# Optimization experiments

Hardware: AMD Instinct MI355X
Metric: run time of the kernel (lower is better)

The kernel has to match this reference:

```python
import jax, jax.numpy as jnp
import numpy as np

K = 3  # kernel size (hardcoded in module defaults; padding=1, stride=1, dilation=1)


def conv2d(x, w, b, pad=1):
    # x: [B,C,H,W], w: [O,C,kh,kw]
    out = jax.lax.conv_general_dilated(
        x, w, window_strides=(1, 1), padding=[(pad, pad), (pad, pad)],
        dimension_numbers=("NCHW", "OIHW", "NCHW"))
    return out + b[None, :, None, None]


def _bilinear_sample(img, py, px):
    # img: [C,H,W]; py, px: [K*K,Ho,Wo] float sample coords.
    # Zero-padded bilinear sampling (matches torchvision deform_conv2d):
    # each of the 4 corner taps contributes 0 if it lies outside the image.
    H, W = img.shape[1], img.shape[2]
    y0 = jnp.floor(py)
    x0 = jnp.floor(px)
    y1, x1 = y0 + 1.0, x0 + 1.0
    wy1 = py - y0
    wy0 = 1.0 - wy1
    wx1 = px - x0
    wx0 = 1.0 - wx1

    def corner(y, x):
        yi = jnp.clip(y.astype(jnp.int32), 0, H - 1)
        xi = jnp.clip(x.astype(jnp.int32), 0, W - 1)
        valid = ((y >= 0) & (y <= H - 1) & (x >= 0) & (x <= W - 1))
        return img[:, yi, xi] * valid.astype(img.dtype)[None]  # [C,K*K,Ho,Wo]

    return (corner(y0, x0) * (wy0 * wx0)[None]
            + corner(y0, x1) * (wy0 * wx1)[None]
            + corner(y1, x0) * (wy1 * wx0)[None]
            + corner(y1, x1) * (wy1 * wx1)[None])


def setup_inputs() -> dict:
    key = jax.random.key(0)
    ks = jax.random.split(key, 4)
    B, C, O, H, W = 8, 128, 256, 96, 96
    x = jax.random.normal(ks[0], (B, C, H, W), dtype=jnp.float32)
    # scale offset/mask conv weights so learned offsets stay a few pixels
    offset_w = jax.random.normal(ks[1], (2 * K * K, C, K, K), dtype=jnp.float32) * 0.01
    offset_b = jnp.zeros((2 * K * K,), dtype=jnp.float32)
    mask_w = jax.random.normal(ks[2], (K * K, C, K, K), dtype=jnp.float32) * 0.05
    mask_b = jnp.zeros((K * K,), dtype=jnp.float32)
    weight = jax.random.normal(ks[3], (O, C, K, K), dtype=jnp.float32) * 0.05
    bias = jnp.zeros((O,), dtype=jnp.float32)
    return {"x": x, "offset_w": offset_w, "offset_b": offset_b,
            "mask_w": mask_w, "mask_b": mask_b, "weight": weight, "bias": bias}


def reference(x, offset_w, offset_b, mask_w, mask_b, weight, bias):
    B, C, H, W = x.shape
    O = weight.shape[0]
    pad = 1
    offset = conv2d(x, offset_w, offset_b, pad)              # [B,2*K*K,H,W]
    mask = jax.nn.sigmoid(conv2d(x, mask_w, mask_b, pad))    # [B,K*K,H,W]
    Ho, Wo = offset.shape[2], offset.shape[3]

    # base sampling grid: output pixel - pad + kernel tap position
    kh, kw = jnp.meshgrid(jnp.arange(K), jnp.arange(K), indexing="ij")
    kh = kh.reshape(-1).astype(x.dtype)  # [K*K]
    kw = kw.reshape(-1).astype(x.dtype)
    base_y = (jnp.arange(Ho, dtype=x.dtype)[None, :, None] - pad
              + kh[:, None, None])                           # [K*K,Ho,1]
    base_x = (jnp.arange(Wo, dtype=x.dtype)[None, None, :] - pad
              + kw[:, None, None])                           # [K*K,1,Wo]

    # torchvision layout: channel 2k = y-offset, 2k+1 = x-offset for tap k
    off = offset.reshape(B, K * K, 2, Ho, Wo)
    py = base_y[None] + off[:, :, 0]                         # [B,K*K,Ho,Wo]
    px = base_x[None] + off[:, :, 1]

    samples = jax.vmap(_bilinear_sample)(x, py, px)          # [B,C,K*K,Ho,Wo]
    w_flat = weight.reshape(O, C, K * K)
    out = jnp.einsum("bckhw,bkhw,ock->bohw", samples, mask, w_flat)
    return out + bias[None, :, None, None]
```

## Files before the change

### kernel.cpp

```cpp
#include <hip/hip_runtime.h>

#define CIN 128
#define COUT 256
#define IH 96
#define IW 96
#define NB 8
#define HW (IH*IW)
#define NPIX (NB*HW)
#define AST 136
#define BLK_PER_IMG (HW/64)

typedef __attribute__((ext_vector_type(8))) short short8;
typedef __attribute__((ext_vector_type(4))) float floatx4;

static __device__ __forceinline__ short f2bf(float f) {
  unsigned int u = __builtin_bit_cast(unsigned int, f);
  u = u + 0x7fffu + ((u >> 16) & 1u);
  return (short)(u >> 16);
}
static __device__ __forceinline__ float bf2f(short s) {
  unsigned int u = ((unsigned int)(unsigned short)s) << 16;
  return __builtin_bit_cast(float, u);
}

struct Corner {
  float w00, w01, w10, w11;
  const short *r00, *r01, *r10, *r11;
};

static __device__ __forceinline__ Corner corner_setup(float py, float px, float mk,
                                                      const short* xtb, int choff) {
  Corner c;
  float y0f = floorf(py), x0f = floorf(px);
  float wy1 = py - y0f, wx1 = px - x0f;
  float wy0 = 1.f - wy1, wx0 = 1.f - wx1;
  bool vy0 = (y0f >= 0.f) && (y0f <= (float)(IH - 1));
  bool vy1 = (y0f + 1.f >= 0.f) && (y0f + 1.f <= (float)(IH - 1));
  bool vx0 = (x0f >= 0.f) && (x0f <= (float)(IW - 1));
  bool vx1 = (x0f + 1.f >= 0.f) && (x0f + 1.f <= (float)(IW - 1));
  int iy0 = min(max((int)y0f, 0), IH - 1);
  int iy1 = min(max((int)y0f + 1, 0), IH - 1);
  int ix0 = min(max((int)x0f, 0), IW - 1);
  int ix1 = min(max((int)x0f + 1, 0), IW - 1);
  c.w00 = wy0 * wx0 * mk * ((vy0 && vx0) ? 1.f : 0.f);
  c.w01 = wy0 * wx1 * mk * ((vy0 && vx1) ? 1.f : 0.f);
  c.w10 = wy1 * wx0 * mk * ((vy1 && vx0) ? 1.f : 0.f);
  c.w11 = wy1 * wx1 * mk * ((vy1 && vx1) ? 1.f : 0.f);
  c.r00 = xtb + (size_t)(iy0 * IW + ix0) * 128 + choff;
  c.r01 = xtb + (size_t)(iy0 * IW + ix1) * 128 + choff;
  c.r10 = xtb + (size_t)(iy1 * IW + ix0) * 128 + choff;
  c.r11 = xtb + (size_t)(iy1 * IW + ix1) * 128 + choff;
  return c;
}

static __device__ __forceinline__ short8 interp8(short8 s00, short8 s01,
                                                 short8 s10, short8 s11,
                                                 const Corner& c) {
  short8 o;
  #pragma unroll
  for (int j = 0; j < 8; ++j) {
    float v = c.w00 * bf2f(s00[j]) + c.w01 * bf2f(s01[j])
            + c.w10 * bf2f(s10[j]) + c.w11 * bf2f(s11[j]);
    o[j] = f2bf(v);
  }
  return o;
}

__global__ void prep_weights(const float* __restrict__ weight,
                             const float* __restrict__ offset_w,
                             const float* __restrict__ mask_w,
                             short* __restrict__ Bt2f,
                             short* __restrict__ Bt1f) {
  int idx = blockIdx.x * 256 + threadIdx.x;
  const int n2 = 9 * 4 * 16 * 512;
  if (idx < n2) {
    int e = idx & 7, lane = (idx >> 3) & 63;
    int g = idx >> 9;
    int nl = g & 15, kq = (g >> 4) & 3, tap = g >> 6;
    int o = nl * 16 + (lane & 15);
    int c = kq * 32 + (lane >> 4) * 8 + e;
    Bt2f[idx] = f2bf(weight[(o * CIN + c) * 9 + tap]);
  } else {
    int j = idx - n2;
    if (j < 9 * 4 * 2 * 512) {
      int e = j & 7, lane = (j >> 3) & 63;
      int g = j >> 9;
      int nl = g & 1, kq = (g >> 1) & 3, tap = g >> 3;
      int n = nl * 16 + (lane & 15);
      int c = kq * 32 + (lane >> 4) * 8 + e;
      float v = 0.f;
      if (n < 27)
        v = (n < 18) ? offset_w[(n * CIN + c) * 9 + tap]
                     : mask_w[((n - 18) * CIN + c) * 9 + tap];
      Bt1f[j] = f2bf(v);
    }
  }
}

__global__ __launch_bounds__(256, 8)
void transpose_x(const float* __restrict__ x, short* __restrict__ xt) {
  __shared__ short tile[64 * 130];
  const int tid = threadIdx.x;
  const int lane = tid & 63;
  const int wv = tid >> 6;
  const int p0 = blockIdx.x * 64;
  const int b = p0 / HW;
  const int hw0 = p0 % HW;
  const float* xb = x + (size_t)b * CIN * HW + hw0;

  #pragma unroll
  for (int i = 0; i < 32; ++i) {
    int c = wv + i * 4;
    tile[lane * 130 + c] = f2bf(xb[(size_t)c * HW + lane]);
  }
  __syncthreads();

  unsigned int* dst = (unsigned int*)(xt + ((size_t)b * HW + hw0) * 128);
  #pragma unroll
  for (int i = 0; i < 16; ++i) {
    int idx = i * 256 + tid;
    int px = idx >> 6, cw = idx & 63;
    unsigned int lo = (unsigned short)tile[px * 130 + 2 * cw];
    unsigned int hi = (unsigned short)tile[px * 130 + 2 * cw + 1];
    dst[idx] = lo | (hi << 16);
  }
}

__global__ __launch_bounds__(256, 4)
void offmask_kernel(const short* __restrict__ xt,
                    const short* __restrict__ Bt1f,
                    const float* __restrict__ offset_b,
                    const float* __restrict__ mask_b,
                    float* __restrict__ pmt) {
  const int tid  = threadIdx.x;
  const int lane = tid & 63;
  const int wv   = tid >> 6;
  const int q    = lane >> 4;
  const int m    = lane & 15;
  const int blk  = blockIdx.x;
  const int l    = (blk & 7) * BLK_PER_IMG + (blk >> 3);
  const int p0   = l * 64;
  const int b    = p0 / HW;
  const int p    = p0 + wv * 16 + m;
  const int hw   = p % HW;
  const int h    = hw / IW, w_ = hw % IW;
  const short* xtb = xt + (size_t)b * HW * 128;

  floatx4 acc0 = (floatx4){0.f, 0.f, 0.f, 0.f};
  floatx4 acc1 = (floatx4){0.f, 0.f, 0.f, 0.f};

  for (int tap = 0; tap < 9; ++tap) {
    const int kh = tap / 3, kw = tap % 3;
    const int iy = h + kh - 1, ix = w_ + kw - 1;
    const bool vald = (iy >= 0 && iy < IH && ix >= 0 && ix < IW);
    const size_t pbase = vald ? (size_t)(iy * IW + ix) * 128 : 0;

    short8 a[4], bb0[4], bb1[4];
    #pragma unroll
    for (int kq = 0; kq < 4; ++kq)
      a[kq] = *(const short8*)(xtb + pbase + kq * 32 + q * 8);
    #pragma unroll
    for (int kq = 0; kq < 4; ++kq) {
      bb0[kq] = *(const short8*)(Bt1f + (size_t)((tap * 4 + kq) * 2 + 0) * 512 + lane * 8);
      bb1[kq] = *(const short8*)(Bt1f + (size_t)((tap * 4 + kq) * 2 + 1) * 512 + lane * 8);
    }
    #pragma unroll
    for (int kq = 0; kq < 4; ++kq) {
      short8 av = a[kq];
      if (!vald) av = (short8){0, 0, 0, 0, 0, 0, 0, 0};
      acc0 = __builtin_amdgcn_mfma_f32_16x16x32_bf16(av, bb0[kq], acc0, 0, 0, 0);
      acc1 = __builtin_amdgcn_mfma_f32_16x16x32_bf16(av, bb1[kq], acc1, 0, 0, 0);
    }
  }

  #pragma unroll
  for (int nl = 0; nl < 2; ++nl) {
    floatx4 ac = nl ? acc1 : acc0;
    int ch = nl * 16 + m;
    if (ch < 18) {
      int tap = ch >> 1, plane = ch & 1;
      float cb = offset_b[ch];
      #pragma unroll
      for (int r = 0; r < 4; ++r) {
        int pp = p0 + wv * 16 + q * 4 + r;
        int hwp = pp % HW;
        float base = plane ? (float)(hwp % IW + tap % 3 - 1)
                           : (float)(hwp / IW + tap / 3 - 1);
        pmt[(size_t)(plane * 9 + tap) * NPIX + pp] = ac[r] + cb + base;
      }
    } else if (ch < 27) {
      int tap = ch - 18;
      float cb = mask_b[tap];
      #pragma unroll
      for (int r = 0; r < 4; ++r) {
        int pp = p0 + wv * 16 + q * 4 + r;
        float v = ac[r] + cb;
        pmt[(size_t)(18 + tap) * NPIX + pp] = 1.f / (1.f + expf(-v));
      }
    }
  }
}

__global__ __launch_bounds__(256, 2)
void deform_main(const short* __restrict__ xt,
                 const short* __restrict__ Bt2f,
                 const float* __restrict__ pmt,
                 const float* __restrict__ bias,
                 float* __restrict__ out) {
  __shared__ short Ald[2][64 * AST];

  const int tid  = threadIdx.x;
  const int lane = tid & 63;
  const int wv   = tid >> 6;
  const int q    = lane >> 4;
  const int m    = lane & 15;
  const int blk  = blockIdx.x;
  const int l    = (blk & 7) * BLK_PER_IMG + (blk >> 3);
  const int p0   = l * 64;
  const int b    = p0 / HW;
  const short* xtb = xt + (size_t)b * HW * 128;

  const int spx   = lane;
  const int p_s   = p0 + spx;
  const int choff = wv * 32;
  const int wsw   = (spx >> 1) & 7;
  const int rsw   = (m >> 1) & 7;
  short* const myrow0 = &Ald[0][spx * AST];
  short* const myrow1 = &Ald[1][spx * AST];

  floatx4 acc[4][4];
  #pragma unroll
  for (int i = 0; i < 4; ++i)
    #pragma unroll
    for (int j = 0; j < 4; ++j) acc[i][j] = (floatx4){0.f, 0.f, 0.f, 0.f};

  {
    float py = pmt[p_s];
    float px = pmt[(size_t)9 * NPIX + p_s];
    float mk = pmt[(size_t)18 * NPIX + p_s];
    Corner c = corner_setup(py, px, mk, xtb, choff);
    #pragma unroll
    for (int i = 0; i < 4; ++i) {
      short8 s00 = *(const short8*)(c.r00 + i * 8);
      short8 s01 = *(const short8*)(c.r01 + i * 8);
      short8 s10 = *(const short8*)(c.r10 + i * 8);
      short8 s11 = *(const short8*)(c.r11 + i * 8);
      *(short8*)(myrow0 + ((wv * 4 + i) ^ wsw) * 8) = interp8(s00, s01, s10, s11, c);
    }
  }
  float pyN = pmt[(size_t)1 * NPIX + p_s];
  float pxN = pmt[(size_t)10 * NPIX + p_s];
  float mkN = pmt[(size_t)19 * NPIX + p_s];
  __syncthreads();

  for (int tap = 0; tap < 9; ++tap) {
    const short* bufr = Ald[tap & 1];
    short* const roww = (tap & 1) ? myrow0 : myrow1;
    const bool nxt = (tap < 8);

    Corner c;
    if (nxt) c = corner_setup(pyN, pxN, mkN, xtb, choff);
    if (tap < 7) {
      pyN = pmt[(size_t)(tap + 2) * NPIX + p_s];
      pxN = pmt[(size_t)(tap + 11) * NPIX + p_s];
      mkN = pmt[(size_t)(tap + 20) * NPIX + p_s];
    }

    short8 bfA[4], bfB[4];
    #pragma unroll
    for (int nl = 0; nl < 4; ++nl) {
      bfA[nl] = *(const short8*)(Bt2f + (size_t)((tap * 4 + 0) * 16 + wv * 4 + nl) * 512 + lane * 8);
      bfB[nl] = *(const short8*)(Bt2f + (size_t)((tap * 4 + 1) * 16 + wv * 4 + nl) * 512 + lane * 8);
    }
    short8 gA0, gA1, gA2, gA3, gB0, gB1, gB2, gB3;
    if (nxt) {
      gA0 = *(const short8*)(c.r00 + 0);  gA1 = *(const short8*)(c.r01 + 0);
      gA2 = *(const short8*)(c.r10 + 0);  gA3 = *(const short8*)(c.r11 + 0);
      gB0 = *(const short8*)(c.r00 + 8);  gB1 = *(const short8*)(c.r01 + 8);
      gB2 = *(const short8*)(c.r10 + 8);  gB3 = *(const short8*)(c.r11 + 8);
    }
    {
      short8 af[4];
      #pragma unroll
      for (int mt = 0; mt < 4; ++mt)
        af[mt] = *(const short8*)(bufr + (mt * 16 + m) * AST + ((0 * 4 + q) ^ rsw) * 8);
      #pragma unroll
      for (int mt = 0; mt < 4; ++mt)
        #pragma unroll
        for (int nl = 0; nl < 4; ++nl)
          acc[mt][nl] = __builtin_amdgcn_mfma_f32_16x16x32_bf16(af[mt], bfA[nl], acc[mt][nl], 0, 0, 0);
    }
    {
      short8 af[4];
      #pragma unroll
      for (int mt = 0; mt < 4; ++mt)
        af[mt] = *(const short8*)(bufr + (mt * 16 + m) * AST + ((1 * 4 + q) ^ rsw) * 8);
      #pragma unroll
      for (int mt = 0; mt < 4; ++mt)
        #pragma unroll
        for (int nl = 0; nl < 4; ++nl)
          acc[mt][nl] = __builtin_amdgcn_mfma_f32_16x16x32_bf16(af[mt], bfB[nl], acc[mt][nl], 0, 0, 0);
    }
    short8 bfC[4], bfD[4];
    #pragma unroll
    for (int nl = 0; nl < 4; ++nl) {
      bfC[nl] = *(const short8*)(Bt2f + (size_t)((tap * 4 + 2) * 16 + wv * 4 + nl) * 512 + lane * 8);
      bfD[nl] = *(const short8*)(Bt2f + (size_t)((tap * 4 + 3) * 16 + wv * 4 + nl) * 512 + lane * 8);
    }
    if (nxt) {
      *(short8*)(roww + ((wv * 4 + 0) ^ wsw) * 8) = interp8(gA0, gA1, gA2, gA3, c);
      *(short8*)(roww + ((wv * 4 + 1) ^ wsw) * 8) = interp8(gB0, gB1, gB2, gB3, c);
      gA0 = *(const short8*)(c.r00 + 16);  gA1 = *(const short8*)(c.r01 + 16);
      gA2 = *(const short8*)(c.r10 + 16);  gA3 = *(const short8*)(c.r11 + 16);
      gB0 = *(const short8*)(c.r00 + 24);  gB1 = *(const short8*)(c.r01 + 24);
      gB2 = *(const short8*)(c.r10 + 24);  gB3 = *(const short8*)(c.r11 + 24);
    }
    {
      short8 af[4];
      #pragma unroll
      for (int mt = 0; mt < 4; ++mt)
        af[mt] = *(const short8*)(bufr + (mt * 16 + m) * AST + ((2 * 4 + q) ^ rsw) * 8);
      #pragma unroll
      for (int mt = 0; mt < 4; ++mt)
        #pragma unroll
        for (int nl = 0; nl < 4; ++nl)
          acc[mt][nl] = __builtin_amdgcn_mfma_f32_16x16x32_bf16(af[mt], bfC[nl], acc[mt][nl], 0, 0, 0);
    }
    {
      short8 af[4];
      #pragma unroll
      for (int mt = 0; mt < 4; ++mt)
        af[mt] = *(const short8*)(bufr + (mt * 16 + m) * AST + ((3 * 4 + q) ^ rsw) * 8);
      #pragma unroll
      for (int mt = 0; mt < 4; ++mt)
        #pragma unroll
        for (int nl = 0; nl < 4; ++nl)
          acc[mt][nl] = __builtin_amdgcn_mfma_f32_16x16x32_bf16(af[mt], bfD[nl], acc[mt][nl], 0, 0, 0);
    }
    if (nxt) {
      *(short8*)(roww + ((wv * 4 + 2) ^ wsw) * 8) = interp8(gA0, gA1, gA2, gA3, c);
      *(short8*)(roww + ((wv * 4 + 3) ^ wsw) * 8) = interp8(gB0, gB1, gB2, gB3, c);
      __syncthreads();
    }
  }

  const int hw0 = p0 % HW;
  #pragma unroll
  for (int nl = 0; nl < 4; ++nl) {
    const int o = wv * 64 + nl * 16 + m;
    const float bs = bias[o];
    float* op = out + (size_t)(b * COUT + o) * HW + hw0;
    #pragma unroll
    for (int mt = 0; mt < 4; ++mt) {
      floatx4 v = acc[mt][nl];
      v[0] += bs; v[1] += bs; v[2] += bs; v[3] += bs;
      *(floatx4*)(op + mt * 16 + q * 4) = v;
    }
  }
}

extern "C" void kernel_launch(void* const* d_in, const int* in_sizes, int n_in,
                              void* d_out, int out_size, void* d_ws, size_t ws_size,
                              hipStream_t stream) {
  const float* x        = (const float*)d_in[0];
  const float* offset_w = (const float*)d_in[1];
  const float* offset_b = (const float*)d_in[2];
  const float* mask_w   = (const float*)d_in[3];
  const float* mask_b   = (const float*)d_in[4];
  const float* weight   = (const float*)d_in[5];
  const float* bias     = (const float*)d_in[6];
  float* out = (float*)d_out;

  char* ws = (char*)d_ws;
  const size_t XT_BYTES  = (size_t)NPIX * 128 * 2;
  const size_t PMT_BYTES = (size_t)27 * NPIX * 4;
  const size_t BT2_BYTES = (size_t)9 * 4 * 16 * 512 * 2;
  short* xtp  = (short*)ws;
  float* pmt  = (float*)(ws + XT_BYTES);
  short* Bt2f = (short*)(ws + XT_BYTES + PMT_BYTES);
  short* Bt1f = (short*)(ws + XT_BYTES + PMT_BYTES + BT2_BYTES);

  prep_weights<<<dim3(1296), dim3(256), 0, stream>>>(weight, offset_w, mask_w, Bt2f, Bt1f);
  transpose_x<<<dim3(NPIX / 64), dim3(256), 0, stream>>>(x, xtp);
  offmask_kernel<<<dim3(NPIX / 64), dim3(256), 0, stream>>>(xtp, Bt1f, offset_b, mask_b, pmt);
  deform_main<<<dim3(NPIX / 64), dim3(256), 0, stream>>>(xtp, Bt2f, pmt, bias, out);
}
```

Measured before the change: 257.3 us.

## Remap gather threads so 8 lanes share a pixel for coalesced channel loads

The bilinear gather is reorganised so that each group of 8 lanes covers one pixel's 128 channels (two 64-channel halves). Each wave now handles 16 pixel rows instead of each lane owning one pixel's 32-channel slice. The goal is contiguous 128-byte global loads per corner instead of scattered per-lane 64-byte segments, which should cut memory transactions in the gather. In exchange each lane does two corner setups per tap, so offset loads and address arithmetic are duplicated across lanes.

```diff
diff --git a/kernel.cpp b/kernel.cpp
--- a/kernel.cpp
+++ b/kernel.cpp
@@ -220,13 +220,18 @@
   const int b    = p0 / HW;
   const short* xtb = xt + (size_t)b * HW * 128;
 
-  const int spx   = lane;
-  const int p_s   = p0 + spx;
-  const int choff = wv * 32;
-  const int wsw   = (spx >> 1) & 7;
+  const int r8    = lane >> 3;
+  const int ck    = lane & 7;
+  const int ckoff = ck * 8;
+  const int row0  = wv * 16 + r8;
+  const int row1  = row0 + 8;
+  const int p_s0  = p0 + row0;
+  const int p_s1  = p0 + row1;
+  const int wk0   = (row0 >> 1) & 7;
+  const int wk1   = (row1 >> 1) & 7;
+  const int wb0   = row0 * AST;
+  const int wb1   = row1 * AST;
   const int rsw   = (m >> 1) & 7;
-  short* const myrow0 = &Ald[0][spx * AST];
-  short* const myrow1 = &Ald[1][spx * AST];
 
   floatx4 acc[4][4];
   #pragma unroll
@@ -235,35 +240,48 @@
     for (int j = 0; j < 4; ++j) acc[i][j] = (floatx4){0.f, 0.f, 0.f, 0.f};
 
   {
-    float py = pmt[p_s];
-    float px = pmt[(size_t)9 * NPIX + p_s];
-    float mk = pmt[(size_t)18 * NPIX + p_s];
-    Corner c = corner_setup(py, px, mk, xtb, choff);
-    #pragma unroll
-    for (int i = 0; i < 4; ++i) {
-      short8 s00 = *(const short8*)(c.r00 + i * 8);
-      short8 s01 = *(const short8*)(c.r01 + i * 8);
-      short8 s10 = *(const short8*)(c.r10 + i * 8);
-      short8 s11 = *(const short8*)(c.r11 + i * 8);
-      *(short8*)(myrow0 + ((wv * 4 + i) ^ wsw) * 8) = interp8(s00, s01, s10, s11, c);
-    }
-  }
-  float pyN = pmt[(size_t)1 * NPIX + p_s];
-  float pxN = pmt[(size_t)10 * NPIX + p_s];
-  float mkN = pmt[(size_t)19 * NPIX + p_s];
+    float py0 = pmt[p_s0], px0 = pmt[(size_t)9 * NPIX + p_s0], mk0 = pmt[(size_t)18 * NPIX + p_s0];
+    float py1 = pmt[p_s1], px1 = pmt[(size_t)9 * NPIX + p_s1], mk1 = pmt[(size_t)18 * NPIX + p_s1];
+    Corner c0 = corner_setup(py0, px0, mk0, xtb, ckoff);
+    Corner c1 = corner_setup(py1, px1, mk1, xtb, ckoff);
+    short8 a0 = *(const short8*)(c0.r00),      a1 = *(const short8*)(c0.r01);
+    short8 a2 = *(const short8*)(c0.r10),      a3 = *(const short8*)(c0.r11);
+    short8 a4 = *(const short8*)(c0.r00 + 64), a5 = *(const short8*)(c0.r01 + 64);
+    short8 a6 = *(const short8*)(c0.r10 + 64), a7 = *(const short8*)(c0.r11 + 64);
+    short8 b0 = *(const short8*)(c1.r00),      b1 = *(const short8*)(c1.r01);
+    short8 b2 = *(const short8*)(c1.r10),      b3 = *(const short8*)(c1.r11);
+    short8 b4 = *(const short8*)(c1.r00 + 64), b5 = *(const short8*)(c1.r01 + 64);
+    short8 b6 = *(const short8*)(c1.r10 + 64), b7 = *(const short8*)(c1.r11 + 64);
+    *(short8*)(&Ald[0][wb0 + (ck ^ wk0) * 8])       = interp8(a0, a1, a2, a3, c0);
+    *(short8*)(&Ald[0][wb0 + (8 + (ck ^ wk0)) * 8]) = interp8(a4, a5, a6, a7, c0);
+    *(short8*)(&Ald[0][wb1 + (ck ^ wk1) * 8])       = interp8(b0, b1, b2, b3, c1);
+    *(short8*)(&Ald[0][wb1 + (8 + (ck ^ wk1)) * 8]) = interp8(b4, b5, b6, b7, c1);
+  }
+  float pyN0 = pmt[(size_t)1 * NPIX + p_s0];
+  float pxN0 = pmt[(size_t)10 * NPIX + p_s0];
+  float mkN0 = pmt[(size_t)19 * NPIX + p_s0];
+  float pyN1 = pmt[(size_t)1 * NPIX + p_s1];
+  float pxN1 = pmt[(size_t)10 * NPIX + p_s1];
+  float mkN1 = pmt[(size_t)19 * NPIX + p_s1];
   __syncthreads();
 
   for (int tap = 0; tap < 9; ++tap) {
     const short* bufr = Ald[tap & 1];
-    short* const roww = (tap & 1) ? myrow0 : myrow1;
+    short* const wbuf = Ald[(tap & 1) ^ 1];
     const bool nxt = (tap < 8);
 
-    Corner c;
-    if (nxt) c = corner_setup(pyN, pxN, mkN, xtb, choff);
+    Corner c0, c1;
+    if (nxt) {
+      c0 = corner_setup(pyN0, pxN0, mkN0, xtb, ckoff);
+      c1 = corner_setup(pyN1, pxN1, mkN1, xtb, ckoff);
+    }
     if (tap < 7) {
-      pyN = pmt[(size_t)(tap + 2) * NPIX + p_s];
-      pxN = pmt[(size_t)(tap + 11) * NPIX + p_s];
-      mkN = pmt[(size_t)(tap + 20) * NPIX + p_s];
+      pyN0 = pmt[(size_t)(tap + 2) * NPIX + p_s0];
+      pxN0 = pmt[(size_t)(tap + 11) * NPIX + p_s0];
+      mkN0 = pmt[(size_t)(tap + 20) * NPIX + p_s0];
+      pyN1 = pmt[(size_t)(tap + 2) * NPIX + p_s1];
+      pxN1 = pmt[(size_t)(tap + 11) * NPIX + p_s1];
+      mkN1 = pmt[(size_t)(tap + 20) * NPIX + p_s1];
     }
 
     short8 bfA[4], bfB[4];
@@ -272,12 +290,12 @@
       bfA[nl] = *(const short8*)(Bt2f + (size_t)((tap * 4 + 0) * 16 + wv * 4 + nl) * 512 + lane * 8);
       bfB[nl] = *(const short8*)(Bt2f + (size_t)((tap * 4 + 1) * 16 + wv * 4 + nl) * 512 + lane * 8);
     }
-    short8 gA0, gA1, gA2, gA3, gB0, gB1, gB2, gB3;
+    short8 g0, g1, g2, g3, g4, g5, g6, g7;
     if (nxt) {
-      gA0 = *(const short8*)(c.r00 + 0);  gA1 = *(const short8*)(c.r01 + 0);
-      gA2 = *(const short8*)(c.r10 + 0);  gA3 = *(const short8*)(c.r11 + 0);
-      gB0 = *(const short8*)(c.r00 + 8);  gB1 = *(const short8*)(c.r01 + 8);
-      gB2 = *(const short8*)(c.r10 + 8);  gB3 = *(const short8*)(c.r11 + 8);
+      g0 = *(const short8*)(c0.r00);      g1 = *(const short8*)(c0.r01);
+      g2 = *(const short8*)(c0.r10);      g3 = *(const short8*)(c0.r11);
+      g4 = *(const short8*)(c0.r00 + 64); g5 = *(const short8*)(c0.r01 + 64);
+      g6 = *(const short8*)(c0.r10 + 64); g7 = *(const short8*)(c0.r11 + 64);
     }
     {
       short8 af[4];
@@ -308,12 +326,12 @@
       bfD[nl] = *(const short8*)(Bt2f + (size_t)((tap * 4 + 3) * 16 + wv * 4 + nl) * 512 + lane * 8);
     }
     if (nxt) {
-      *(short8*)(roww + ((wv * 4 + 0) ^ wsw) * 8) = interp8(gA0, gA1, gA2, gA3, c);
-      *(short8*)(roww + ((wv * 4 + 1) ^ wsw) * 8) = interp8(gB0, gB1, gB2, gB3, c);
-      gA0 = *(const short8*)(c.r00 + 16);  gA1 = *(const short8*)(c.r01 + 16);
-      gA2 = *(const short8*)(c.r10 + 16);  gA3 = *(const short8*)(c.r11 + 16);
-      gB0 = *(const short8*)(c.r00 + 24);  gB1 = *(const short8*)(c.r01 + 24);
-      gB2 = *(const short8*)(c.r10 + 24);  gB3 = *(const short8*)(c.r11 + 24);
+      *(short8*)(&wbuf[wb0 + (ck ^ wk0) * 8])       = interp8(g0, g1, g2, g3, c0);
+      *(short8*)(&wbuf[wb0 + (8 + (ck ^ wk0)) * 8]) = interp8(g4, g5, g6, g7, c0);
+      g0 = *(const short8*)(c1.r00);      g1 = *(const short8*)(c1.r01);
+      g2 = *(const short8*)(c1.r10);      g3 = *(const short8*)(c1.r11);
+      g4 = *(const short8*)(c1.r00 + 64); g5 = *(const short8*)(c1.r01 + 64);
+      g6 = *(const short8*)(c1.r10 + 64); g7 = *(const short8*)(c1.r11 + 64);
     }
     {
       short8 af[4];
@@ -338,8 +356,8 @@
           acc[mt][nl] = __builtin_amdgcn_mfma_f32_16x16x32_bf16(af[mt], bfD[nl], acc[mt][nl], 0, 0, 0);
     }
     if (nxt) {
-      *(short8*)(roww + ((wv * 4 + 2) ^ wsw) * 8) = interp8(gA0, gA1, gA2, gA3, c);
-      *(short8*)(roww + ((wv * 4 + 3) ^ wsw) * 8) = interp8(gB0, gB1, gB2, gB3, c);
+      *(short8*)(&wbuf[wb1 + (ck ^ wk1) * 8])       = interp8(g0, g1, g2, g3, c1);
+      *(short8*)(&wbuf[wb1 + (8 + (ck ^ wk1)) * 8]) = interp8(g4, g5, g6, g7, c1);
       __syncthreads();
     }
   }
```

New measurement: 225.6 us. -12.3%, faster.
